# Kernel tuning notes

Measured on AMD Instinct MI355X. Metric: run time of the kernel, lower is better.

Reference implementation:

```python
import jax, jax.numpy as jnp
import numpy as np

NUM_KERNELS = 6
ALPHA = 0.5
DIL = 9
FEAT = 4
DELTA_V = 0.5
DELTA_D = 1.5
EMB_W = 0.25
MAX_LABELS = 16


def setup_inputs() -> dict:
    key = jax.random.key(0)
    k1, k2, k3, k4, k5 = jax.random.split(key, 5)
    B, H, W = 8, 640, 640
    pred = jax.random.normal(k1, (B, NUM_KERNELS + FEAT, H, W), dtype=jnp.float32)
    gt_text = (jax.random.uniform(k2, (B, 1, H, W)) < 0.3).astype(jnp.float32)
    gt_kernels = (jax.random.uniform(k3, (B, NUM_KERNELS - 1, H, W)) < 0.2).astype(jnp.float32)
    training_mask = (jax.random.uniform(k4, (B, 1, H, W)) > 0.05).astype(jnp.float32)
    gt_instance = jax.random.randint(k5, (B, H, W), 0, MAX_LABELS, dtype=jnp.int32)
    return {"pred": pred, "gt_text": gt_text, "gt_kernels": gt_kernels,
            "training_mask": training_mask, "gt_instance": gt_instance}


def _dice(inp, tgt, msk, eps=1e-6):
    # inp/tgt/msk: [N, HW]; returns mean over N of (1 - 2*I/U)
    inp = inp * msk
    tgt = tgt * msk
    inter = (inp * tgt).sum(1)
    union = (inp ** 2).sum(1) + (tgt ** 2).sum(1) + eps
    return (1.0 - 2.0 * inter / union).mean()


def _ohem(pred, gt, tm, ratio=3):
    # Vectorized OHEM: keep all positives + top-(3*n_pos) hardest negatives per sample.
    B = gt.shape[0]
    p = pred.reshape(B, -1)
    g = gt.reshape(B, -1)
    m = tm.reshape(B, -1)
    pos = (g > 0.5) & (m > 0.5)
    neg = (g <= 0.5) & (m > 0.5)
    n_pos = pos.sum(1)
    n_neg = jnp.minimum(ratio * n_pos, neg.sum(1))
    score = jnp.where(neg, p, -jnp.inf)
    # rank[i,j] = position of element j in descending order of score[i]
    rank = jnp.argsort(jnp.argsort(-score, axis=1), axis=1)
    mask = pos | (neg & (rank < n_neg[:, None]))
    return mask.astype(pred.dtype).reshape(gt.shape)


def _emb_sample(emb, gt, tm):
    # emb: [D,H,W], gt: [H,W] int, tm: [H,W]
    D = emb.shape[0]
    e = emb.reshape(D, -1).T                       # [HW, D]
    g = gt.reshape(-1)
    valid = tm.reshape(-1) > 0
    ids = jnp.where(valid, g, MAX_LABELS)          # invalid pixels -> dump segment
    ones = valid.astype(e.dtype)
    counts = jax.ops.segment_sum(ones, ids, num_segments=MAX_LABELS + 1)[:MAX_LABELS]
    sums = jax.ops.segment_sum(e * ones[:, None], ids, num_segments=MAX_LABELS + 1)[:MAX_LABELS]
    present = counts > 0
    n = present.sum()
    nf = n.astype(e.dtype)
    means = sums / jnp.maximum(counts, 1.0)[:, None]   # [L, D]
    # variance term: per-pixel distance to own cluster mean
    own = means[g]                                     # [HW, D]
    d = jnp.sqrt(((e - own) ** 2).sum(1) + 1e-12)
    cv = jnp.maximum(d - DELTA_V, 0.0) ** 2
    per = jax.ops.segment_sum(cv * ones, ids, num_segments=MAX_LABELS + 1)[:MAX_LABELS]
    per = per / jnp.maximum(counts, 1.0)
    lv = jnp.where(present, per, 0.0).sum() / jnp.maximum(nf, 1.0)
    # distance term: pairwise over present cluster means (unordered pairs i<j)
    diff = means[:, None, :] - means[None, :, :]
    pd = jnp.sqrt((diff ** 2).sum(-1) + 1e-12)
    iu = jnp.arange(MAX_LABELS)
    pm = present[:, None] & present[None, :] & (iu[:, None] < iu[None, :])
    ld = jnp.where(pm, jnp.maximum(2.0 * DELTA_D - pd, 0.0) ** 2, 0.0).sum()
    ld = ld / jnp.maximum(nf * (nf - 1.0), 1.0)
    # regularization: mean norm of present cluster means
    lr = jnp.where(present, jnp.sqrt((means ** 2).sum(1) + 1e-12), 0.0).sum() / jnp.maximum(nf, 1.0)
    act = (n > 1).astype(e.dtype)   # skip samples with <=1 instance (matches `continue`)
    return act * lv, act * ld, act * lr


def reference(pred, gt_text, gt_kernels, training_mask, gt_instance):
    B = pred.shape[0]
    gt_t = gt_text[:, 0]
    tm = training_mask[:, 0]
    # text branch: sigmoid -> 9x9 max-pool dilation -> OHEM dice
    prob = jax.nn.sigmoid(pred[:, 0])
    pad = DIL // 2
    dil = jax.lax.reduce_window(prob, -jnp.inf, jax.lax.max,
                                (1, DIL, DIL), (1, 1, 1),
                                [(0, 0), (pad, pad), (pad, pad)])
    ohem = jax.lax.stop_gradient(_ohem(dil, gt_t, tm, ratio=3))
    loss_text = _dice(dil.reshape(B, -1), gt_t.reshape(B, -1), ohem.reshape(B, -1))
    # kernel branch: mean over (B, K) equals sum_k dice_k / K
    K = NUM_KERNELS - 1
    pk = jax.nn.sigmoid(pred[:, 1:NUM_KERNELS]).reshape(B * K, -1)
    gk = gt_kernels.reshape(B * K, -1)
    mk = jnp.broadcast_to(tm[:, None], (B, K) + tm.shape[1:]).reshape(B * K, -1)
    loss_kernels = _dice(pk, gk, mk)
    # embedding clustering loss
    pred_emb = pred[:, NUM_KERNELS:]
    lv, ld, lr = jax.vmap(_emb_sample)(pred_emb, gt_instance, tm)
    loss_emb = EMB_W * (lv.sum() + ld.sum() + 0.001 * (lr.sum() / B))
    loss = loss_kernels + ALPHA * loss_text + loss_emb
    return loss, loss_text, loss_kernels, loss_emb
```

## Files before the change

### kernel.cpp

```cpp
#include <hip/hip_runtime.h>
#include <math.h>

#define BB 8
#define HH 640
#define WW 640
#define HWN (HH*WW)
#define CC 10
#define KCH 5
#define DD 4
#define LL 16
#define NBINS 256

#define WS_OHEM      0
#define WS_HCNT      64
#define WS_HS2       (WS_HCNT + BB*NBINS)
#define WS_KERN      (WS_HS2 + BB*NBINS)
#define WS_ECNT      (WS_KERN + 120)
#define WS_ESUM      (WS_ECNT + BB*LL)
#define WS_ECV       (WS_ESUM + BB*LL*DD)
#define WS_ZERO_END  (WS_ECV + BB*LL)
#define WS_MEANS     WS_ZERO_END
#define WS_MISC      (WS_MEANS + BB*LL*DD)

__device__ __forceinline__ float sigm(float x) { return 1.f / (1.f + expf(-x)); }

__device__ __forceinline__ float wave_red(float v) {
    #pragma unroll
    for (int o = 32; o > 0; o >>= 1) v += __shfl_down(v, o);
    return v;
}

__global__ __launch_bounds__(256) void k_dil_stats(
    const float* __restrict__ pred, const float* __restrict__ gt_t,
    const float* __restrict__ tm, float* __restrict__ ws)
{
    __shared__ float tile[40][41];
    __shared__ float hmax[40][33];
    __shared__ float hcnt[NBINS];
    __shared__ float hs2[NBINS];
    __shared__ float red[8];
    const int b  = blockIdx.z;
    const int x0 = blockIdx.x * 32 - 4;
    const int y0 = blockIdx.y * 32 - 4;
    const int tid = threadIdx.y * 32 + threadIdx.x;
    const float* p0 = pred + (size_t)b * CC * HWN;

    for (int i = tid; i < NBINS; i += 256) { hcnt[i] = 0.f; hs2[i] = 0.f; }
    if (tid < 8) red[tid] = 0.f;

    for (int i = tid; i < 40 * 40; i += 256) {
        int r = i / 40, c = i - r * 40;
        int gy = y0 + r, gx = x0 + c;
        float v = -INFINITY;
        if (gy >= 0 && gy < HH && gx >= 0 && gx < WW) v = p0[gy * WW + gx];
        tile[r][c] = v;
    }
    __syncthreads();
    for (int i = tid; i < 40 * 32; i += 256) {
        int r = i >> 5, c = i & 31;
        float m = tile[r][c];
        #pragma unroll
        for (int k = 1; k < 9; k++) m = fmaxf(m, tile[r][c + k]);
        hmax[r][c] = m;
    }
    __syncthreads();

    float c_pos = 0.f, s_pos = 0.f, s_pos2 = 0.f, c_neg = 0.f, s_neg2 = 0.f;
    const int cx = threadIdx.x;
    for (int ry = threadIdx.y; ry < 32; ry += 8) {
        float m = hmax[ry][cx];
        #pragma unroll
        for (int k = 1; k < 9; k++) m = fmaxf(m, hmax[ry + k][cx]);
        float dil = sigm(m);
        int gy = y0 + 4 + ry, gx = x0 + 4 + cx;
        size_t gidx = (size_t)b * HWN + (size_t)gy * WW + gx;
        float g = gt_t[gidx], mv = tm[gidx];
        if (mv > 0.5f) {
            if (g > 0.5f) { c_pos += 1.f; s_pos += dil; s_pos2 += dil * dil; }
            else {
                c_neg += 1.f; s_neg2 += dil * dil;
                int bin = (int)((m + 8.f) * 16.f);
                bin = min(max(bin, 0), NBINS - 1);
                atomicAdd(&hcnt[bin], 1.f);
                atomicAdd(&hs2[bin], dil * dil);
            }
        }
    }
    c_pos = wave_red(c_pos); s_pos = wave_red(s_pos); s_pos2 = wave_red(s_pos2);
    c_neg = wave_red(c_neg); s_neg2 = wave_red(s_neg2);
    if ((tid & 63) == 0) {
        atomicAdd(&red[0], c_pos);  atomicAdd(&red[1], s_pos);
        atomicAdd(&red[2], s_pos2); atomicAdd(&red[3], c_neg);
        atomicAdd(&red[4], s_neg2);
    }
    __syncthreads();
    float* oh = ws + WS_OHEM + b * 8;
    if (tid < 5) atomicAdd(&oh[tid], red[tid]);
    float* gh_c = ws + WS_HCNT + b * NBINS;
    float* gh_s = ws + WS_HS2  + b * NBINS;
    for (int i = tid; i < NBINS; i += 256) {
        if (hcnt[i] != 0.f) { atomicAdd(&gh_c[i], hcnt[i]); atomicAdd(&gh_s[i], hs2[i]); }
    }
}

__global__ __launch_bounds__(256) void k_kern_dice(
    const float* __restrict__ pred, const float* __restrict__ gtk,
    const float* __restrict__ tm, float* __restrict__ ws)
{
    const int row = blockIdx.y;
    const int b = row / KCH, k = row - b * KCH;
    const float4* p = (const float4*)(pred + ((size_t)b * CC + 1 + k) * HWN);
    const float4* g = (const float4*)(gtk + (size_t)row * HWN);
    const float4* m = (const float4*)(tm + (size_t)b * HWN);
    const int nv = HWN / 4;
    float i1 = 0.f, i2 = 0.f, i3 = 0.f;
    for (int j = blockIdx.x * 256 + threadIdx.x; j < nv; j += gridDim.x * 256) {
        float4 pv = p[j], gv = g[j], mv = m[j];
        float s0 = sigm(pv.x), s1 = sigm(pv.y), s2 = sigm(pv.z), s3 = sigm(pv.w);
        i1 += s0*gv.x*mv.x + s1*gv.y*mv.y + s2*gv.z*mv.z + s3*gv.w*mv.w;
        i2 += s0*s0*mv.x + s1*s1*mv.y + s2*s2*mv.z + s3*s3*mv.w;
        i3 += gv.x*mv.x + gv.y*mv.y + gv.z*mv.z + gv.w*mv.w;
    }
    i1 = wave_red(i1); i2 = wave_red(i2); i3 = wave_red(i3);
    __shared__ float sred[12];
    int wv = threadIdx.x >> 6;
    if ((threadIdx.x & 63) == 0) { sred[wv*3] = i1; sred[wv*3+1] = i2; sred[wv*3+2] = i3; }
    __syncthreads();
    if (threadIdx.x == 0) {
        float a = 0.f, bb = 0.f, c = 0.f;
        for (int w = 0; w < 4; w++) { a += sred[w*3]; bb += sred[w*3+1]; c += sred[w*3+2]; }
        float* kk = ws + WS_KERN + row * 3;
        atomicAdd(&kk[0], a); atomicAdd(&kk[1], bb); atomicAdd(&kk[2], c);
    }
}

__global__ __launch_bounds__(256) void k_emb1(
    const float* __restrict__ pred, const int* __restrict__ inst,
    const float* __restrict__ tm, float* __restrict__ ws)
{
    const int b = blockIdx.y;
    const int tid = threadIdx.x;
    const float* e0 = pred + ((size_t)b * CC + 6) * HWN;
    const float4* v0p = (const float4*)e0;
    const float4* v1p = (const float4*)(e0 + HWN);
    const float4* v2p = (const float4*)(e0 + 2 * HWN);
    const float4* v3p = (const float4*)(e0 + 3 * HWN);
    const float4* tmv = (const float4*)(tm + (size_t)b * HWN);
    const int4*   iv  = (const int4*)(inst + (size_t)b * HWN);

    float cnt[LL], s0[LL], s1[LL], s2[LL], s3[LL];
    #pragma unroll
    for (int l = 0; l < LL; l++) { cnt[l]=0.f; s0[l]=0.f; s1[l]=0.f; s2[l]=0.f; s3[l]=0.f; }

    const int nv = HWN / 4;
    for (int j = blockIdx.x * 256 + tid; j < nv; j += gridDim.x * 256) {
        float4 a0 = v0p[j], a1 = v1p[j], a2 = v2p[j], a3 = v3p[j];
        float4 t = tmv[j];
        int4 li = iv[j];
        int lab0 = (t.x > 0.f) ? li.x : LL;
        int lab1 = (t.y > 0.f) ? li.y : LL;
        int lab2 = (t.z > 0.f) ? li.z : LL;
        int lab3 = (t.w > 0.f) ? li.w : LL;
        #pragma unroll
        for (int l = 0; l < LL; l++) {
            float m0 = (lab0 == l) ? 1.f : 0.f;
            float m1 = (lab1 == l) ? 1.f : 0.f;
            float m2 = (lab2 == l) ? 1.f : 0.f;
            float m3 = (lab3 == l) ? 1.f : 0.f;
            cnt[l] += (m0 + m1) + (m2 + m3);
            s0[l] += m0*a0.x + m1*a0.y + m2*a0.z + m3*a0.w;
            s1[l] += m0*a1.x + m1*a1.y + m2*a1.z + m3*a1.w;
            s2[l] += m0*a2.x + m1*a2.y + m2*a2.z + m3*a2.w;
            s3[l] += m0*a3.x + m1*a3.y + m2*a3.z + m3*a3.w;
        }
    }

    __shared__ float sred[4][80];
    const int wv = tid >> 6, ln = tid & 63;
    #pragma unroll
    for (int l = 0; l < LL; l++) {
        float r0 = wave_red(cnt[l]);
        float r1 = wave_red(s0[l]);
        float r2 = wave_red(s1[l]);
        float r3 = wave_red(s2[l]);
        float r4 = wave_red(s3[l]);
        if (ln == 0) {
            sred[wv][l*5+0] = r0; sred[wv][l*5+1] = r1; sred[wv][l*5+2] = r2;
            sred[wv][l*5+3] = r3; sred[wv][l*5+4] = r4;
        }
    }
    __syncthreads();
    if (tid < 80) {
        float s = sred[0][tid] + sred[1][tid] + sred[2][tid] + sred[3][tid];
        int l = tid / 5, c = tid - l * 5;
        if (c == 0) atomicAdd(&ws[WS_ECNT + b * LL + l], s);
        else        atomicAdd(&ws[WS_ESUM + b * LL * DD + l * DD + (c - 1)], s);
    }
}

__global__ __launch_bounds__(128) void k_emb_means(float* __restrict__ ws)
{
    const int b = blockIdx.x;
    __shared__ float mn[LL][DD];
    __shared__ float pres[LL];
    __shared__ float redp[128];
    __shared__ float redr[LL];
    const int tid = threadIdx.x;
    if (tid < LL) {
        float c = ws[WS_ECNT + b * LL + tid];
        float inv = 1.f / fmaxf(c, 1.f);
        #pragma unroll
        for (int d = 0; d < DD; d++) {
            float mv = ws[WS_ESUM + b * LL * DD + tid * DD + d] * inv;
            mn[tid][d] = mv;
            ws[WS_MEANS + b * LL * DD + tid * DD + d] = mv;
        }
        pres[tid] = (c > 0.f) ? 1.f : 0.f;
    }
    __syncthreads();
    float ldv = 0.f;
    if (tid < 120) {
        int idx = tid, ii = 0;
        while (idx >= (LL - 1 - ii)) { idx -= (LL - 1 - ii); ii++; }
        int jj = ii + 1 + idx;
        float s = 1e-12f;
        #pragma unroll
        for (int d = 0; d < DD; d++) { float df = mn[ii][d] - mn[jj][d]; s += df * df; }
        float pd = sqrtf(s);
        float t = fmaxf(3.0f - pd, 0.f);
        ldv = (pres[ii] > 0.f && pres[jj] > 0.f) ? t * t : 0.f;
    }
    redp[tid] = ldv;
    float lrv = 0.f;
    if (tid < LL && pres[tid] > 0.f) {
        float s = 1e-12f;
        #pragma unroll
        for (int d = 0; d < DD; d++) s += mn[tid][d] * mn[tid][d];
        lrv = sqrtf(s);
    }
    if (tid < LL) redr[tid] = lrv;
    __syncthreads();
    if (tid == 0) {
        float nf = 0.f;
        for (int i = 0; i < LL; i++) nf += pres[i];
        float ld = 0.f;
        for (int i = 0; i < 120; i++) ld += redp[i];
        float lr = 0.f;
        for (int i = 0; i < LL; i++) lr += redr[i];
        float act = (nf > 1.f) ? 1.f : 0.f;
        ld = act * ld / fmaxf(nf * (nf - 1.f), 1.f);
        lr = act * lr / fmaxf(nf, 1.f);
        ws[WS_MISC + b * 4 + 0] = nf;
        ws[WS_MISC + b * 4 + 1] = ld;
        ws[WS_MISC + b * 4 + 2] = lr;
        ws[WS_MISC + b * 4 + 3] = act;
    }
}

__global__ __launch_bounds__(256) void k_emb2(
    const float* __restrict__ pred, const int* __restrict__ inst,
    const float* __restrict__ tm, float* __restrict__ ws)
{
    const int b = blockIdx.y;
    const int tid = threadIdx.x;
    __shared__ float mn[LL * DD];
    if (tid < LL * DD) mn[tid] = ws[WS_MEANS + b * LL * DD + tid];
    __syncthreads();

    const float* e0 = pred + ((size_t)b * CC + 6) * HWN;
    const float4* v0p = (const float4*)e0;
    const float4* v1p = (const float4*)(e0 + HWN);
    const float4* v2p = (const float4*)(e0 + 2 * HWN);
    const float4* v3p = (const float4*)(e0 + 3 * HWN);
    const float4* tmv = (const float4*)(tm + (size_t)b * HWN);
    const int4*   iv  = (const int4*)(inst + (size_t)b * HWN);

    float cv[LL];
    #pragma unroll
    for (int l = 0; l < LL; l++) cv[l] = 0.f;

    const int nv = HWN / 4;
    for (int j = blockIdx.x * 256 + tid; j < nv; j += gridDim.x * 256) {
        float4 a0 = v0p[j], a1 = v1p[j], a2 = v2p[j], a3 = v3p[j];
        float4 t = tmv[j];
        int4 li = iv[j];
        int lab[4];
        lab[0] = (t.x > 0.f) ? li.x : LL;
        lab[1] = (t.y > 0.f) ? li.y : LL;
        lab[2] = (t.z > 0.f) ? li.z : LL;
        lab[3] = (t.w > 0.f) ? li.w : LL;
        float ex[4] = {a0.x, a0.y, a0.z, a0.w};
        float ey[4] = {a1.x, a1.y, a1.z, a1.w};
        float ez[4] = {a2.x, a2.y, a2.z, a2.w};
        float ew[4] = {a3.x, a3.y, a3.z, a3.w};
        #pragma unroll
        for (int q = 0; q < 4; q++) {
            int l = lab[q];
            int lc = (l < LL) ? l : 0;
            float d0 = ex[q] - mn[lc * DD + 0];
            float d1 = ey[q] - mn[lc * DD + 1];
            float d2 = ez[q] - mn[lc * DD + 2];
            float d3 = ew[q] - mn[lc * DD + 3];
            float dd = sqrtf(d0*d0 + d1*d1 + d2*d2 + d3*d3 + 1e-12f);
            float tt = fmaxf(dd - 0.5f, 0.f);
            float t2 = tt * tt;
            #pragma unroll
            for (int k = 0; k < LL; k++) {
                float m = (l == k) ? 1.f : 0.f;
                cv[k] += m * t2;
            }
        }
    }

    __shared__ float sred[4][LL];
    const int wv = tid >> 6, ln = tid & 63;
    #pragma unroll
    for (int l = 0; l < LL; l++) {
        float r = wave_red(cv[l]);
        if (ln == 0) sred[wv][l] = r;
    }
    __syncthreads();
    if (tid < LL) {
        float s = sred[0][tid] + sred[1][tid] + sred[2][tid] + sred[3][tid];
        atomicAdd(&ws[WS_ECV + b * LL + tid], s);
    }
}

__global__ __launch_bounds__(64) void k_final(const float* __restrict__ ws, float* __restrict__ out)
{
    __shared__ float s_text[BB];
    __shared__ float s_kern[40];
    __shared__ float s_lv[BB], s_ld[BB], s_lr[BB];
    const int tid = threadIdx.x;
    if (tid < BB) {
        const float* o = ws + WS_OHEM + tid * 8;
        float npos = o[0], spos = o[1], spos2 = o[2], nnegt = o[3], sneg2t = o[4];
        float nneg = fminf(3.f * npos, nnegt);
        float ssel;
        if (nneg >= nnegt) ssel = sneg2t;
        else {
            const float* hc = ws + WS_HCNT + tid * NBINS;
            const float* hs = ws + WS_HS2  + tid * NBINS;
            float acc = 0.f; ssel = 0.f;
            for (int i = NBINS - 1; i >= 0; i--) {
                float c = hc[i];
                if (c <= 0.f) continue;
                if (acc + c <= nneg) { ssel += hs[i]; acc += c; }
                else { float r = nneg - acc; ssel += r * (hs[i] / c); break; }
            }
        }
        float uni = spos2 + ssel + npos + 1e-6f;
        s_text[tid] = 1.f - 2.f * spos / uni;

        float nf  = ws[WS_MISC + tid * 4 + 0];
        float act = ws[WS_MISC + tid * 4 + 3];
        float lv = 0.f;
        for (int l = 0; l < LL; l++) {
            float c = ws[WS_ECNT + tid * LL + l];
            if (c > 0.f) lv += ws[WS_ECV + tid * LL + l] / fmaxf(c, 1.f);
        }
        s_lv[tid] = act * lv / fmaxf(nf, 1.f);
        s_ld[tid] = ws[WS_MISC + tid * 4 + 1];
        s_lr[tid] = ws[WS_MISC + tid * 4 + 2];
    }
    if (tid < 40) {
        const float* kk = ws + WS_KERN + tid * 3;
        s_kern[tid] = 1.f - 2.f * kk[0] / (kk[1] + kk[2] + 1e-6f);
    }
    __syncthreads();
    if (tid == 0) {
        float lt = 0.f; for (int i = 0; i < BB; i++) lt += s_text[i]; lt /= (float)BB;
        float lk = 0.f; for (int i = 0; i < 40; i++) lk += s_kern[i]; lk /= 40.f;
        float lvs = 0.f, lds_ = 0.f, lrs = 0.f;
        for (int i = 0; i < BB; i++) { lvs += s_lv[i]; lds_ += s_ld[i]; lrs += s_lr[i]; }
        float lemb = 0.25f * (lvs + lds_ + 0.001f * (lrs / (float)BB));
        out[0] = lk + 0.5f * lt + lemb;
        out[1] = lt;
        out[2] = lk;
        out[3] = lemb;
    }
}

extern "C" void kernel_launch(void* const* d_in, const int* in_sizes, int n_in,
                              void* d_out, int out_size, void* d_ws, size_t ws_size,
                              hipStream_t stream)
{
    (void)in_sizes; (void)n_in; (void)out_size; (void)ws_size;
    const float* pred = (const float*)d_in[0];
    const float* gt_t = (const float*)d_in[1];
    const float* gtk  = (const float*)d_in[2];
    const float* tm   = (const float*)d_in[3];
    const int*   inst = (const int*)d_in[4];
    float* out = (float*)d_out;
    float* ws  = (float*)d_ws;

    hipMemsetAsync(d_ws, 0, WS_ZERO_END * sizeof(float), stream);

    dim3 g1(WW / 32, HH / 32, BB), b1(32, 8, 1);
    k_dil_stats<<<g1, b1, 0, stream>>>(pred, gt_t, tm, ws);
    k_kern_dice<<<dim3(32, 40), 256, 0, stream>>>(pred, gtk, tm, ws);
    k_emb1<<<dim3(64, BB), 256, 0, stream>>>(pred, inst, tm, ws);
    k_emb_means<<<BB, 128, 0, stream>>>(ws);
    k_emb2<<<dim3(64, BB), 256, 0, stream>>>(pred, inst, tm, ws);
    k_final<<<1, 64, 0, stream>>>(ws, out);
}
```

Baseline: 349.1 us.

## Retile dilation to 64x64 with vector row-max, simplify emb2 accumulation, resize grids

The dilation kernel moves to 64x64 tiles. It builds the horizontal 9-wide max straight from vectorized global float4 loads using prefix/suffix max, which drops the raw shared tile and one sync. It also splits the shared histograms in two to reduce atomic contention. The variance kernel now premultiplies by per-label inverse counts and keeps a single scalar accumulator instead of 16 per-label registers and 16 wave reductions. Grid sizes for the kernel-dice and embedding kernels are increased for more parallelism. Larger tiles lower the block count and may reduce occupancy in the dilation kernel.

New measurement: 354.8 us. Within noise of the previous version (+1.7%).

```diff
diff --git a/kernel.cpp b/kernel.cpp
--- a/kernel.cpp
+++ b/kernel.cpp
@@ -18,9 +18,10 @@
 #define WS_ECNT      (WS_KERN + 120)
 #define WS_ESUM      (WS_ECNT + BB*LL)
 #define WS_ECV       (WS_ESUM + BB*LL*DD)
-#define WS_ZERO_END  (WS_ECV + BB*LL)
+#define WS_ZERO_END  (WS_ECV + BB)
 #define WS_MEANS     WS_ZERO_END
-#define WS_MISC      (WS_MEANS + BB*LL*DD)
+#define WS_INVC      (WS_MEANS + BB*LL*DD)
+#define WS_MISC      (WS_INVC + BB*LL)
 
 __device__ __forceinline__ float sigm(float x) { return 1.f / (1.f + expf(-x)); }
 
@@ -30,50 +31,73 @@
     return v;
 }
 
+__device__ __forceinline__ float4 ld4g(const float* __restrict__ p, int row, int cb) {
+    float4 v;
+    if (row < 0 || row >= HH) { v.x = v.y = v.z = v.w = -INFINITY; return v; }
+    const float* rp = p + (size_t)row * WW;
+    if (cb >= 0 && cb <= WW - 4) return *(const float4*)(rp + cb);
+    v.x = ((unsigned)(cb + 0) < (unsigned)WW) ? rp[cb + 0] : -INFINITY;
+    v.y = ((unsigned)(cb + 1) < (unsigned)WW) ? rp[cb + 1] : -INFINITY;
+    v.z = ((unsigned)(cb + 2) < (unsigned)WW) ? rp[cb + 2] : -INFINITY;
+    v.w = ((unsigned)(cb + 3) < (unsigned)WW) ? rp[cb + 3] : -INFINITY;
+    return v;
+}
+
 __global__ __launch_bounds__(256) void k_dil_stats(
     const float* __restrict__ pred, const float* __restrict__ gt_t,
     const float* __restrict__ tm, float* __restrict__ ws)
 {
-    __shared__ float tile[40][41];
-    __shared__ float hmax[40][33];
-    __shared__ float hcnt[NBINS];
-    __shared__ float hs2[NBINS];
+    __shared__ float hmax[72][65];
+    __shared__ float hcnt[2][NBINS];
+    __shared__ float hs2[2][NBINS];
     __shared__ float red[8];
     const int b  = blockIdx.z;
-    const int x0 = blockIdx.x * 32 - 4;
-    const int y0 = blockIdx.y * 32 - 4;
-    const int tid = threadIdx.y * 32 + threadIdx.x;
+    const int x0 = blockIdx.x * 64;
+    const int y0 = blockIdx.y * 64;
+    const int tid = threadIdx.x;
     const float* p0 = pred + (size_t)b * CC * HWN;
 
-    for (int i = tid; i < NBINS; i += 256) { hcnt[i] = 0.f; hs2[i] = 0.f; }
+    for (int i = tid; i < 2 * NBINS; i += 256) {
+        ((float*)hcnt)[i] = 0.f; ((float*)hs2)[i] = 0.f;
+    }
     if (tid < 8) red[tid] = 0.f;
 
-    for (int i = tid; i < 40 * 40; i += 256) {
-        int r = i / 40, c = i - r * 40;
-        int gy = y0 + r, gx = x0 + c;
-        float v = -INFINITY;
-        if (gy >= 0 && gy < HH && gx >= 0 && gx < WW) v = p0[gy * WW + gx];
-        tile[r][c] = v;
-    }
-    __syncthreads();
-    for (int i = tid; i < 40 * 32; i += 256) {
-        int r = i >> 5, c = i & 31;
-        float m = tile[r][c];
-        #pragma unroll
-        for (int k = 1; k < 9; k++) m = fmaxf(m, tile[r][c + k]);
-        hmax[r][c] = m;
-    }
-    __syncthreads();
-
+    for (int i = tid; i < 72 * 16; i += 256) {
+        int r = i >> 4, g = i & 15;
+        int gr = y0 + r - 4;
+        int cb = x0 + 4 * g - 4;
+        float4 A = ld4g(p0, gr, cb);
+        float4 Bv = ld4g(p0, gr, cb + 4);
+        float4 Cv = ld4g(p0, gr, cb + 8);
+        float s3 = A.w;
+        float s2 = fmaxf(A.z, s3);
+        float s1 = fmaxf(A.y, s2);
+        float s0 = fmaxf(A.x, s1);
+        float mid = fmaxf(fmaxf(Bv.x, Bv.y), fmaxf(Bv.z, Bv.w));
+        float q0 = Cv.x;
+        float q1 = fmaxf(q0, Cv.y);
+        float q2 = fmaxf(q1, Cv.z);
+        float q3 = fmaxf(q2, Cv.w);
+        int c = 4 * g;
+        hmax[r][c + 0] = fmaxf(fmaxf(s0, mid), q0);
+        hmax[r][c + 1] = fmaxf(fmaxf(s1, mid), q1);
+        hmax[r][c + 2] = fmaxf(fmaxf(s2, mid), q2);
+        hmax[r][c + 3] = fmaxf(fmaxf(s3, mid), q3);
+    }
+    __syncthreads();
+
+    const int c  = tid & 63;
+    const int rb = tid >> 6;
+    const int hc = tid >> 7;
     float c_pos = 0.f, s_pos = 0.f, s_pos2 = 0.f, c_neg = 0.f, s_neg2 = 0.f;
-    const int cx = threadIdx.x;
-    for (int ry = threadIdx.y; ry < 32; ry += 8) {
-        float m = hmax[ry][cx];
-        #pragma unroll
-        for (int k = 1; k < 9; k++) m = fmaxf(m, hmax[ry + k][cx]);
+    #pragma unroll
+    for (int k = 0; k < 16; k++) {
+        int r = rb * 16 + k;
+        float m = hmax[r][c];
+        #pragma unroll
+        for (int j = 1; j < 9; j++) m = fmaxf(m, hmax[r + j][c]);
         float dil = sigm(m);
-        int gy = y0 + 4 + ry, gx = x0 + 4 + cx;
-        size_t gidx = (size_t)b * HWN + (size_t)gy * WW + gx;
+        size_t gidx = (size_t)b * HWN + (size_t)(y0 + r) * WW + (x0 + c);
         float g = gt_t[gidx], mv = tm[gidx];
         if (mv > 0.5f) {
             if (g > 0.5f) { c_pos += 1.f; s_pos += dil; s_pos2 += dil * dil; }
@@ -81,8 +105,8 @@
                 c_neg += 1.f; s_neg2 += dil * dil;
                 int bin = (int)((m + 8.f) * 16.f);
                 bin = min(max(bin, 0), NBINS - 1);
-                atomicAdd(&hcnt[bin], 1.f);
-                atomicAdd(&hs2[bin], dil * dil);
+                atomicAdd(&hcnt[hc][bin], 1.f);
+                atomicAdd(&hs2[hc][bin], dil * dil);
             }
         }
     }
@@ -99,7 +123,11 @@
     float* gh_c = ws + WS_HCNT + b * NBINS;
     float* gh_s = ws + WS_HS2  + b * NBINS;
     for (int i = tid; i < NBINS; i += 256) {
-        if (hcnt[i] != 0.f) { atomicAdd(&gh_c[i], hcnt[i]); atomicAdd(&gh_s[i], hs2[i]); }
+        float sc = hcnt[0][i] + hcnt[1][i];
+        if (sc != 0.f) {
+            atomicAdd(&gh_c[i], sc);
+            atomicAdd(&gh_s[i], hs2[0][i] + hs2[1][i]);
+        }
     }
 }
 
@@ -209,6 +237,7 @@
     if (tid < LL) {
         float c = ws[WS_ECNT + b * LL + tid];
         float inv = 1.f / fmaxf(c, 1.f);
+        ws[WS_INVC + b * LL + tid] = inv;
         #pragma unroll
         for (int d = 0; d < DD; d++) {
             float mv = ws[WS_ESUM + b * LL * DD + tid * DD + d] * inv;
@@ -264,7 +293,9 @@
     const int b = blockIdx.y;
     const int tid = threadIdx.x;
     __shared__ float mn[LL * DD];
+    __shared__ float invc[LL];
     if (tid < LL * DD) mn[tid] = ws[WS_MEANS + b * LL * DD + tid];
+    if (tid < LL) invc[tid] = ws[WS_INVC + b * LL + tid];
     __syncthreads();
 
     const float* e0 = pred + ((size_t)b * CC + 6) * HWN;
@@ -275,55 +306,39 @@
     const float4* tmv = (const float4*)(tm + (size_t)b * HWN);
     const int4*   iv  = (const int4*)(inst + (size_t)b * HWN);
 
-    float cv[LL];
-    #pragma unroll
-    for (int l = 0; l < LL; l++) cv[l] = 0.f;
-
+    float acc = 0.f;
     const int nv = HWN / 4;
     for (int j = blockIdx.x * 256 + tid; j < nv; j += gridDim.x * 256) {
         float4 a0 = v0p[j], a1 = v1p[j], a2 = v2p[j], a3 = v3p[j];
         float4 t = tmv[j];
         int4 li = iv[j];
-        int lab[4];
-        lab[0] = (t.x > 0.f) ? li.x : LL;
-        lab[1] = (t.y > 0.f) ? li.y : LL;
-        lab[2] = (t.z > 0.f) ? li.z : LL;
-        lab[3] = (t.w > 0.f) ? li.w : LL;
         float ex[4] = {a0.x, a0.y, a0.z, a0.w};
         float ey[4] = {a1.x, a1.y, a1.z, a1.w};
         float ez[4] = {a2.x, a2.y, a2.z, a2.w};
         float ew[4] = {a3.x, a3.y, a3.z, a3.w};
+        int   lb[4] = {li.x, li.y, li.z, li.w};
+        float tv[4] = {t.x, t.y, t.z, t.w};
         #pragma unroll
         for (int q = 0; q < 4; q++) {
-            int l = lab[q];
-            int lc = (l < LL) ? l : 0;
-            float d0 = ex[q] - mn[lc * DD + 0];
-            float d1 = ey[q] - mn[lc * DD + 1];
-            float d2 = ez[q] - mn[lc * DD + 2];
-            float d3 = ew[q] - mn[lc * DD + 3];
+            int l = lb[q];
+            float d0 = ex[q] - mn[l * DD + 0];
+            float d1 = ey[q] - mn[l * DD + 1];
+            float d2 = ez[q] - mn[l * DD + 2];
+            float d3 = ew[q] - mn[l * DD + 3];
             float dd = sqrtf(d0*d0 + d1*d1 + d2*d2 + d3*d3 + 1e-12f);
             float tt = fmaxf(dd - 0.5f, 0.f);
-            float t2 = tt * tt;
-            #pragma unroll
-            for (int k = 0; k < LL; k++) {
-                float m = (l == k) ? 1.f : 0.f;
-                cv[k] += m * t2;
-            }
-        }
-    }
-
-    __shared__ float sred[4][LL];
-    const int wv = tid >> 6, ln = tid & 63;
-    #pragma unroll
-    for (int l = 0; l < LL; l++) {
-        float r = wave_red(cv[l]);
-        if (ln == 0) sred[wv][l] = r;
-    }
-    __syncthreads();
-    if (tid < LL) {
-        float s = sred[0][tid] + sred[1][tid] + sred[2][tid] + sred[3][tid];
-        atomicAdd(&ws[WS_ECV + b * LL + tid], s);
-    }
+            float w = (tv[q] > 0.f) ? invc[l] : 0.f;
+            acc += w * tt * tt;
+        }
+    }
+
+    acc = wave_red(acc);
+    __shared__ float sred[4];
+    const int wv = tid >> 6;
+    if ((tid & 63) == 0) sred[wv] = acc;
+    __syncthreads();
+    if (tid == 0)
+        atomicAdd(&ws[WS_ECV + b], sred[0] + sred[1] + sred[2] + sred[3]);
 }
 
 __global__ __launch_bounds__(64) void k_final(const float* __restrict__ ws, float* __restrict__ out)
@@ -339,11 +354,11 @@
         float ssel;
         if (nneg >= nnegt) ssel = sneg2t;
         else {
-            const float* hc = ws + WS_HCNT + tid * NBINS;
+            const float* hcn = ws + WS_HCNT + tid * NBINS;
             const float* hs = ws + WS_HS2  + tid * NBINS;
             float acc = 0.f; ssel = 0.f;
             for (int i = NBINS - 1; i >= 0; i--) {
-                float c = hc[i];
+                float c = hcn[i];
                 if (c <= 0.f) continue;
                 if (acc + c <= nneg) { ssel += hs[i]; acc += c; }
                 else { float r = nneg - acc; ssel += r * (hs[i] / c); break; }
@@ -354,12 +369,7 @@
 
         float nf  = ws[WS_MISC + tid * 4 + 0];
         float act = ws[WS_MISC + tid * 4 + 3];
-        float lv = 0.f;
-        for (int l = 0; l < LL; l++) {
-            float c = ws[WS_ECNT + tid * LL + l];
-            if (c > 0.f) lv += ws[WS_ECV + tid * LL + l] / fmaxf(c, 1.f);
-        }
-        s_lv[tid] = act * lv / fmaxf(nf, 1.f);
+        s_lv[tid] = act * ws[WS_ECV + tid] / fmaxf(nf, 1.f);
         s_ld[tid] = ws[WS_MISC + tid * 4 + 1];
         s_lr[tid] = ws[WS_MISC + tid * 4 + 2];
     }
@@ -396,11 +406,11 @@
 
     hipMemsetAsync(d_ws, 0, WS_ZERO_END * sizeof(float), stream);
 
-    dim3 g1(WW / 32, HH / 32, BB), b1(32, 8, 1);
+    dim3 g1(WW / 64, HH / 64, BB), b1(256, 1, 1);
     k_dil_stats<<<g1, b1, 0, stream>>>(pred, gt_t, tm, ws);
-    k_kern_dice<<<dim3(32, 40), 256, 0, stream>>>(pred, gtk, tm, ws);
-    k_emb1<<<dim3(64, BB), 256, 0, stream>>>(pred, inst, tm, ws);
+    k_kern_dice<<<dim3(48, 40), 256, 0, stream>>>(pred, gtk, tm, ws);
+    k_emb1<<<dim3(96, BB), 256, 0, stream>>>(pred, inst, tm, ws);
     k_emb_means<<<BB, 128, 0, stream>>>(ws);
-    k_emb2<<<dim3(64, BB), 256, 0, stream>>>(pred, inst, tm, ws);
+    k_emb2<<<dim3(128, BB), 256, 0, stream>>>(pred, inst, tm, ws);
     k_final<<<1, 64, 0, stream>>>(ws, out);
 }
```
